# Kernel tuning notes

Hardware: AMD Instinct MI355X
Metric: run time of the kernel (lower is better)

## Reference

```python
import jax, jax.numpy as jnp
import numpy as np

H = 16
D_K = 64
D_V = 64


def setup_inputs() -> dict:
    key = jax.random.key(0)
    k0, k1, k2, k3, k4 = jax.random.split(key, 5)
    n, l, d_model = 4, 2048, 1024
    s = 1.0 / np.sqrt(d_model)
    Z = jax.random.normal(k0, (n, l, d_model), dtype=jnp.float32)
    mask = jnp.ones((n, 1, 1, l), dtype=jnp.int32)
    Wv = jax.random.normal(k1, (d_model, d_model), dtype=jnp.float32) * s
    Wk = jax.random.normal(k2, (d_model, H * D_K), dtype=jnp.float32) * s
    Wq = jax.random.normal(k3, (d_model, H * D_K), dtype=jnp.float32) * s
    Wo = jax.random.normal(k4, (H * D_V, d_model), dtype=jnp.float32) * s
    return {"Z": Z, "mask": mask, "Wv": Wv, "Wk": Wk, "Wq": Wq, "Wo": Wo}


def reference(Z, mask, Wv, Wk, Wq, Wo):
    n, l, d_model = Z.shape
    values = (Z @ Wv).reshape(n, l, H, D_V)
    keys = (Z @ Wk).reshape(n, l, H, D_K)
    queries = (Z @ Wq).reshape(n, l, H, D_K)
    # dense score matrix [n, h, q, k]
    C = jnp.einsum('nqhd,nkhd->nhqk', queries, keys)
    masked_C = jnp.where(mask == 0, -jnp.inf, C)
    idx = jnp.argmax(masked_C, axis=3)          # [n, h, q] hard top-1 index
    # torch einsum 'nhll,nlhd->nlhd' takes the diagonal of the one-hot
    # scattered C_tilde: diag element is C[n,h,l,l] iff argmax at query l is l.
    diag_C = jnp.einsum('nhll->nhl', C)         # [n, h, l]
    w = jnp.where(idx == jnp.arange(l)[None, None, :], diag_C, 0.0)  # [n, h, l]
    y_bar = (w.transpose(0, 2, 1)[..., None] * values).reshape(n, l, H * D_V)
    return y_bar @ Wo
```

## Files before the change

kernel.cpp:

```cpp
#include <hip/hip_runtime.h>
#include <hip/hip_bf16.h>
#include <string.h>

#define NB   4
#define LSEQ 2048
#define DMODEL 1024
#define NHEAD 16
#define DKH  64
#define CAND_CAP 32768

typedef __attribute__((ext_vector_type(8)))  short          short8v;
typedef __attribute__((ext_vector_type(8)))  unsigned short ushort8v;
typedef __attribute__((ext_vector_type(4)))  unsigned int   uint4v;
typedef __attribute__((ext_vector_type(16))) float          f32x16;

__device__ inline unsigned short bf16_rne(float v) {
  unsigned u = __builtin_bit_cast(unsigned, v);
  unsigned r = u + 0x7FFFu + ((u >> 16) & 1u);
  return (unsigned short)(r >> 16);
}
__device__ inline float bf16_to_f32(unsigned short u) {
  return __builtin_bit_cast(float, (unsigned)u << 16);
}
__device__ inline unsigned cvtpk2(float lo, float hi) {
  __hip_bfloat162 t = __float22bfloat162_rn(float2{lo, hi});
  unsigned u;
  memcpy(&u, &t, 4);
  return u;
}

__global__ __launch_bounds__(256) void wconv(
    const float* __restrict__ Wq, const float* __restrict__ Wk,
    unsigned short* __restrict__ WThi) {
  __shared__ float T[64][65];
  const int col0 = blockIdx.x * 64, k0 = blockIdx.y * 64;
  const float* W = (col0 < 1024) ? Wq : Wk;
  const int cl0 = (col0 < 1024) ? col0 : col0 - 1024;
  const int tid = threadIdx.x;
#pragma unroll
  for (int u = 0; u < 16; ++u) {
    int lin = u * 256 + tid;
    int r = lin >> 6, c = lin & 63;
    T[r][c] = W[(size_t)(k0 + r) * 1024 + cl0 + c];
  }
  __syncthreads();
#pragma unroll
  for (int u = 0; u < 16; ++u) {
    int lin = u * 256 + tid;
    int cc = lin >> 6, kk = lin & 63;
    WThi[(size_t)(col0 + cc) * 1024 + k0 + kk] = bf16_rne(T[kk][cc]);
  }
}

__global__ __launch_bounds__(256) void proj_hi(
    const float* __restrict__ Z, const unsigned short* __restrict__ WThi,
    unsigned short* __restrict__ Qhd, unsigned short* __restrict__ Khd) {
  __shared__ unsigned short As[128 * 64];
  __shared__ unsigned short Bs[128 * 64];
  const int tid = threadIdx.x;
  const int lane = tid & 63, w = tid >> 6;
  const int l31 = lane & 31, half = lane >> 5;
  const int wrow = w >> 1, wcol = w & 1;
  const int bid = blockIdx.x;
  const int xcd = bid & 7, t = bid >> 3;
  const int brow = (xcd * 8 + (t & 7)) * 128;
  const int bcol = (t >> 3) * 128;

  int ar[4], as_[4];
#pragma unroll
  for (int u = 0; u < 4; ++u) { int c = u * 256 + tid; ar[u] = c >> 3; as_[u] = c & 7; }

  const float* Zb = Z + (size_t)brow * 1024;
  const unsigned short* Wb = WThi + (size_t)bcol * 1024;

  float4 raf[4][2];
  ushort8v rb[4];
#pragma unroll
  for (int u = 0; u < 4; ++u) {
    const float* p = Zb + (size_t)ar[u] * 1024 + as_[u] * 8;
    raf[u][0] = *(const float4*)p; raf[u][1] = *(const float4*)(p + 4);
    rb[u] = *(const ushort8v*)(Wb + (size_t)ar[u] * 1024 + as_[u] * 8);
  }

  f32x16 acc[2][2];
#pragma unroll
  for (int m = 0; m < 2; ++m)
#pragma unroll
    for (int nf = 0; nf < 2; ++nf)
#pragma unroll
      for (int r = 0; r < 16; ++r) acc[m][nf][r] = 0.f;

  for (int k0 = 0; k0 < 1024; k0 += 64) {
    __syncthreads();
#pragma unroll
    for (int u = 0; u < 4; ++u) {
      uint4v uv;
      uv[0] = cvtpk2(raf[u][0].x, raf[u][0].y);
      uv[1] = cvtpk2(raf[u][0].z, raf[u][0].w);
      uv[2] = cvtpk2(raf[u][1].x, raf[u][1].y);
      uv[3] = cvtpk2(raf[u][1].z, raf[u][1].w);
      ushort8v h8 = __builtin_bit_cast(ushort8v, uv);
      int r = ar[u], s = as_[u];
      *(ushort8v*)((char*)As + r * 128 + ((s ^ (r & 7)) << 4)) = h8;
      *(ushort8v*)((char*)Bs + r * 128 + ((s ^ (r & 7)) << 4)) = rb[u];
    }
    __syncthreads();
    const int kn = k0 + 64;
    if (kn < 1024) {
#pragma unroll
      for (int u = 0; u < 4; ++u) {
        const float* p = Zb + (size_t)ar[u] * 1024 + kn + as_[u] * 8;
        raf[u][0] = *(const float4*)p; raf[u][1] = *(const float4*)(p + 4);
        rb[u] = *(const ushort8v*)(Wb + (size_t)ar[u] * 1024 + kn + as_[u] * 8);
      }
    }
    short8v aH[2][4], bH[2][4];
#pragma unroll
    for (int m = 0; m < 2; ++m) {
      int r = wrow * 64 + m * 32 + l31;
#pragma unroll
      for (int kc = 0; kc < 4; ++kc) {
        int sh = kc * 2 + half;
        aH[m][kc] = *(const short8v*)((char*)As + r * 128 + ((sh ^ (r & 7)) << 4));
      }
    }
#pragma unroll
    for (int nf = 0; nf < 2; ++nf) {
      int r = wcol * 64 + nf * 32 + l31;
#pragma unroll
      for (int kc = 0; kc < 4; ++kc) {
        int sh = kc * 2 + half;
        bH[nf][kc] = *(const short8v*)((char*)Bs + r * 128 + ((sh ^ (r & 7)) << 4));
      }
    }
#pragma unroll
    for (int m = 0; m < 2; ++m)
#pragma unroll
      for (int nf = 0; nf < 2; ++nf)
#pragma unroll
        for (int kc = 0; kc < 4; ++kc)
          acc[m][nf] = __builtin_amdgcn_mfma_f32_32x32x16_bf16(aH[m][kc], bH[nf][kc], acc[m][nf], 0, 0, 0);
  }

  unsigned short* Out;
  int coff;
  if (bcol < 1024) { Out = Qhd; coff = bcol; } else { Out = Khd; coff = bcol - 1024; }
#pragma unroll
  for (int m = 0; m < 2; ++m)
#pragma unroll
    for (int nf = 0; nf < 2; ++nf) {
      int colg = coff + wcol * 64 + nf * 32 + l31;
      int head = colg >> 6, cin = colg & 63;
#pragma unroll
      for (int r = 0; r < 16; ++r) {
        int rowg = brow + wrow * 64 + m * 32 + (r & 3) + 8 * (r >> 2) + 4 * half;
        int n = rowg >> 11, l = rowg & 2047;
        Out[((size_t)(n * 16 + head) * 2048 + l) * 64 + cin] = bf16_rne(acc[m][nf][r]);
      }
    }
}

__global__ __launch_bounds__(256) void score_hi(
    const unsigned short* __restrict__ Qhd, const unsigned short* __restrict__ Khd,
    int* __restrict__ cnt_cand, int* __restrict__ cand) {
  __shared__ unsigned short Ks[2 * 64 * 128];
  const int tid = threadIdx.x;
  const int lane = tid & 63, w = tid >> 6;
  const int l31 = lane & 31, half = lane >> 5;
  const int bid = blockIdx.x;
  const int xcd = bid & 7, j = bid >> 3;
  const int nh = xcd + 8 * (j >> 4);
  const int qi = j & 15;
  const int n = nh >> 4, h = nh & 15;
  const int qw = qi * 128 + w * 32;

  const unsigned short* qrow = Qhd + ((size_t)(nh) * 2048 + qw + l31) * 64;
  short8v aQ[4];
#pragma unroll
  for (int ds = 0; ds < 4; ++ds)
    aQ[ds] = *(const short8v*)(qrow + ds * 16 + 8 * half);

  f32x16 zac;
#pragma unroll
  for (int r = 0; r < 16; ++r) zac[r] = 0.f;

  float maxO[16], diag[16];
#pragma unroll
  for (int r = 0; r < 16; ++r) { maxO[r] = -3.0e38f; diag[r] = -3.0e38f; }

  const unsigned short* kb = Khd + (size_t)nh * 2048 * 64;
  ushort8v rv[4];
#pragma unroll
  for (int u = 0; u < 4; ++u) {
    int c = u * 256 + tid;
    rv[u] = *(const ushort8v*)(kb + (size_t)(c >> 3) * 64 + (c & 7) * 8);
  }

  for (int kt = 0; kt < LSEQ; kt += 128) {
    char* buf = (char*)Ks + ((kt >> 7) & 1) * 16384;
#pragma unroll
    for (int u = 0; u < 4; ++u) {
      int c = u * 256 + tid;
      int pr = c >> 4, sl = c & 15;
      *(ushort8v*)(buf + pr * 256 + ((sl ^ (pr & 15)) << 4)) = rv[u];
    }
    __syncthreads();
    const int ktn = kt + 128;
    if (ktn < LSEQ) {
#pragma unroll
      for (int u = 0; u < 4; ++u) {
        int c = u * 256 + tid;
        rv[u] = *(const ushort8v*)(kb + (size_t)(ktn + (c >> 3)) * 64 + (c & 7) * 8);
      }
    }
    if (kt == qi * 128) {
#pragma unroll
      for (int ct = 0; ct < 4; ++ct) {
        const int rr = ct * 32 + l31;
        const int pr = rr >> 1;
        short8v bh[4];
#pragma unroll
        for (int ds = 0; ds < 4; ++ds) {
          int sl = ((rr & 1) << 3) | (2 * ds + half);
          bh[ds] = *(const short8v*)(buf + pr * 256 + ((sl ^ (pr & 15)) << 4));
        }
        f32x16 acc = __builtin_amdgcn_mfma_f32_32x32x16_bf16(aQ[0], bh[0], zac, 0, 0, 0);
#pragma unroll
        for (int ds = 1; ds < 4; ++ds)
          acc = __builtin_amdgcn_mfma_f32_32x32x16_bf16(aQ[ds], bh[ds], acc, 0, 0, 0);
        if (ct == w) {
#pragma unroll
          for (int r = 0; r < 16; ++r) {
            const int rloc = (r & 3) + 8 * (r >> 2) + 4 * half;
            if (l31 == rloc) diag[r] = acc[r];
            else             maxO[r] = fmaxf(maxO[r], acc[r]);
          }
        } else {
#pragma unroll
          for (int r = 0; r < 16; ++r) maxO[r] = fmaxf(maxO[r], acc[r]);
        }
      }
    } else {
#pragma unroll
      for (int p = 0; p < 2; ++p) {
        const int rrA = (2 * p) * 32 + l31, rrB = (2 * p + 1) * 32 + l31;
        const int prA = rrA >> 1, prB = rrB >> 1;
        short8v bA[4], bB[4];
#pragma unroll
        for (int ds = 0; ds < 4; ++ds) {
          int slA = ((rrA & 1) << 3) | (2 * ds + half);
          int slB = ((rrB & 1) << 3) | (2 * ds + half);
          bA[ds] = *(const short8v*)(buf + prA * 256 + ((slA ^ (prA & 15)) << 4));
          bB[ds] = *(const short8v*)(buf + prB * 256 + ((slB ^ (prB & 15)) << 4));
        }
        f32x16 accA = __builtin_amdgcn_mfma_f32_32x32x16_bf16(aQ[0], bA[0], zac, 0, 0, 0);
        f32x16 accB = __builtin_amdgcn_mfma_f32_32x32x16_bf16(aQ[0], bB[0], zac, 0, 0, 0);
#pragma unroll
        for (int ds = 1; ds < 4; ++ds) {
          accA = __builtin_amdgcn_mfma_f32_32x32x16_bf16(aQ[ds], bA[ds], accA, 0, 0, 0);
          accB = __builtin_amdgcn_mfma_f32_32x32x16_bf16(aQ[ds], bB[ds], accB, 0, 0, 0);
        }
#pragma unroll
        for (int r = 0; r < 16; ++r)
          maxO[r] = fmaxf(fmaxf(accA[r], accB[r]), maxO[r]);
      }
    }
  }

#pragma unroll
  for (int r = 0; r < 16; ++r) {
    float mo = maxO[r], dg = diag[r];
#pragma unroll
    for (int off = 16; off >= 1; off >>= 1) {
      mo = fmaxf(mo, __shfl_xor(mo, off));
      dg = fmaxf(dg, __shfl_xor(dg, off));
    }
    if (l31 == 0) {
      if (dg >= mo - 0.8f) {
        const int q = qw + (r & 3) + 8 * (r >> 2) + 4 * half;
        int slot = atomicAdd(cnt_cand, 1);
        if (slot < CAND_CAP) cand[slot] = (n << 15) | (h << 11) | q;
      }
    }
  }
}

__global__ __launch_bounds__(256) void recheck2(
    const float* __restrict__ Z, const float* __restrict__ Wq,
    const float* __restrict__ Wk, const float* __restrict__ Wv,
    const float* __restrict__ Wo, const unsigned short* __restrict__ Khd,
    const int* __restrict__ cnt_cand, const int* __restrict__ cand,
    float* __restrict__ out) {
  __shared__ float Zs[1024];
  __shared__ float part[4][64];
  __shared__ float Qex[64];
  __shared__ float Kex[64];
  __shared__ float Svals[2048];
  __shared__ float red[4];
  __shared__ int   Elist[64];
  __shared__ int   Ecnt;
  const int tid = threadIdx.x;
  const int lane = tid & 63, w = tid >> 6;
  int nc = *cnt_cand; if (nc > CAND_CAP) nc = CAND_CAP;

  for (int e = blockIdx.x; e < nc; e += gridDim.x) {
    const int pk = cand[e];
    const int n = pk >> 15, h = (pk >> 11) & 15, q = pk & 2047;
    __syncthreads();
#pragma unroll
    for (int u = 0; u < 4; ++u)
      Zs[tid + u * 256] = Z[((size_t)(n * LSEQ + q)) * 1024 + tid + u * 256];
    if (tid == 0) Ecnt = 0;
    __syncthreads();
    {
      int o = tid & 63, seg = tid >> 6;
      float p = 0.f;
      int d0 = seg * 256;
      for (int d = d0; d < d0 + 256; ++d) p += Zs[d] * Wq[(size_t)d * 1024 + h * 64 + o];
      part[seg][o] = p;
    }
    __syncthreads();
    if (tid < 64) Qex[tid] = part[0][tid] + part[1][tid] + part[2][tid] + part[3][tid];
    __syncthreads();
    const unsigned short* kb = Khd + (size_t)(n * 16 + h) * 2048 * 64;
    float mymax = -3.0e38f;
    for (int k = tid; k < LSEQ; k += 256) {
      const unsigned short* kr = kb + (size_t)k * 64;
      float s = 0.f;
#pragma unroll
      for (int jj = 0; jj < 8; ++jj) {
        ushort8v v = *(const ushort8v*)(kr + jj * 8);
#pragma unroll
        for (int ee = 0; ee < 8; ++ee) s += Qex[jj * 8 + ee] * bf16_to_f32(v[ee]);
      }
      Svals[k] = s;
      if (k != q) mymax = fmaxf(mymax, s);
    }
#pragma unroll
    for (int off = 32; off >= 1; off >>= 1) mymax = fmaxf(mymax, __shfl_xor(mymax, off));
    if (lane == 0) red[w] = mymax;
    __syncthreads();
    const float Mt = fmaxf(fmaxf(red[0], red[1]), fmaxf(red[2], red[3]));
    const float Sqt = Svals[q];
    if (Sqt < Mt - 0.4f) continue;
    for (int k = tid; k < LSEQ; k += 256) {
      if (k != q && Svals[k] >= Sqt - 0.4f) {
        int sl = atomicAdd(&Ecnt, 1);
        if (sl < 64) Elist[sl] = k;
      }
    }
    __syncthreads();
    const int nE = (Ecnt < 64) ? Ecnt : 64;
    float Sq_ex = 0.f;
    bool ok = true;
    for (int i = 0; i <= nE; ++i) {
      const int kk = (i == 0) ? q : Elist[i - 1];
      __syncthreads();
#pragma unroll
      for (int u = 0; u < 4; ++u)
        Zs[tid + u * 256] = Z[((size_t)(n * LSEQ + kk)) * 1024 + tid + u * 256];
      __syncthreads();
      {
        int o = tid & 63, seg = tid >> 6;
        float p = 0.f;
        int d0 = seg * 256;
        for (int d = d0; d < d0 + 256; ++d) p += Zs[d] * Wk[(size_t)d * 1024 + h * 64 + o];
        part[seg][o] = p;
      }
      __syncthreads();
      if (tid < 64) Kex[tid] = part[0][tid] + part[1][tid] + part[2][tid] + part[3][tid];
      __syncthreads();
      if (w == 0) {
        float pr = Qex[lane] * Kex[lane];
#pragma unroll
        for (int off = 32; off >= 1; off >>= 1) pr += __shfl_xor(pr, off);
        if (lane == 0) red[0] = pr;
      }
      __syncthreads();
      const float Sk = red[0];
      if (i == 0) Sq_ex = Sk;
      else        ok = ok && (kk < q ? (Sk < Sq_ex) : (Sk <= Sq_ex));
      __syncthreads();
    }
    if (!ok) continue;
    __syncthreads();
#pragma unroll
    for (int u = 0; u < 4; ++u)
      Zs[tid + u * 256] = Z[((size_t)(n * LSEQ + q)) * 1024 + tid + u * 256];
    __syncthreads();
    {
      int o = tid & 63, seg = tid >> 6;
      float p = 0.f;
      int d0 = seg * 256;
      for (int d = d0; d < d0 + 256; ++d) p += Zs[d] * Wv[(size_t)d * 1024 + h * 64 + o];
      part[seg][o] = p;
    }
    __syncthreads();
    if (tid < 64) Kex[tid] = part[0][tid] + part[1][tid] + part[2][tid] + part[3][tid];
    __syncthreads();
    {
      float a4[4] = {0.f, 0.f, 0.f, 0.f};
      const float* wo = Wo + (size_t)h * DKH * DMODEL;
      for (int jj = 0; jj < 64; ++jj) {
        float vj = Kex[jj];
#pragma unroll
        for (int u = 0; u < 4; ++u) a4[u] += vj * wo[(size_t)jj * DMODEL + tid + u * 256];
      }
      float* orow = out + ((size_t)n * LSEQ + q) * DMODEL;
#pragma unroll
      for (int u = 0; u < 4; ++u) atomicAdd(&orow[tid + u * 256], Sq_ex * a4[u]);
    }
  }
}

extern "C" void kernel_launch(void* const* d_in, const int* in_sizes, int n_in,
                              void* d_out, int out_size, void* d_ws, size_t ws_size,
                              hipStream_t stream) {
  const float* Z  = (const float*)d_in[0];
  const float* Wv = (const float*)d_in[2];
  const float* Wk = (const float*)d_in[3];
  const float* Wq = (const float*)d_in[4];
  const float* Wo = (const float*)d_in[5];
  float* out = (float*)d_out;

  int* cnt_cand = (int*)d_ws;
  int* cand = (int*)((char*)d_ws + 64);
  unsigned short* Khd  = (unsigned short*)((char*)d_ws + (size_t)(4 << 20));
  unsigned short* WThi = (unsigned short*)((char*)d_ws + (size_t)(24 << 20));
  unsigned short* Qhd  = (unsigned short*)d_out;

  hipMemsetAsync(d_ws, 0, 64, stream);

  dim3 gw(32, 16);
  wconv<<<gw, 256, 0, stream>>>(Wq, Wk, WThi);

  proj_hi<<<1024, 256, 0, stream>>>(Z, WThi, Qhd, Khd);

  score_hi<<<1024, 256, 0, stream>>>(Qhd, Khd, cnt_cand, cand);

  hipMemsetAsync(d_out, 0, (size_t)out_size * sizeof(float), stream);
  recheck2<<<256, 256, 0, stream>>>(Z, Wq, Wk, Wv, Wo, Khd, cnt_cand, cand, out);
}
```

Before: 179.6 us.

## Pre-convert Z to bf16 and stage GEMM/score tiles via direct global-to-LDS loads

Adds a zconv kernel that converts Z to bf16 once, then rewrites proj_hi to load A/B tiles with global_load_lds (direct global-to-LDS DMA), using a K-step of 32 and a new XOR swizzle. score_hi also drops its register-staged double buffer in favour of direct LDS loads into a single buffer. The goal is to remove the VGPR round trip and in-loop fp32-to-bf16 conversion, and to cut LDS footprint so occupancy can rise. The cost is an extra kernel pass over Z, twice as many sync-bounded iterations in proj_hi, and the loss of load/compute overlap in score_hi.

```diff
diff --git a/kernel.cpp b/kernel.cpp
--- a/kernel.cpp
+++ b/kernel.cpp
@@ -27,6 +27,22 @@
   unsigned u;
   memcpy(&u, &t, 4);
   return u;
+}
+__device__ inline void gload_lds16(const void* g, void* l) {
+  __builtin_amdgcn_global_load_lds((const __attribute__((address_space(1))) void*)g,
+                                   (__attribute__((address_space(3))) void*)l, 16, 0, 0);
+}
+
+__global__ __launch_bounds__(256) void zconv(
+    const float* __restrict__ Z, unsigned short* __restrict__ Zbf) {
+  size_t c = ((size_t)blockIdx.x * 256 + threadIdx.x) * 8;
+  float4 a = *(const float4*)(Z + c), b = *(const float4*)(Z + c + 4);
+  uint4v uv;
+  uv[0] = cvtpk2(a.x, a.y);
+  uv[1] = cvtpk2(a.z, a.w);
+  uv[2] = cvtpk2(b.x, b.y);
+  uv[3] = cvtpk2(b.z, b.w);
+  *(ushort8v*)(Zbf + c) = __builtin_bit_cast(ushort8v, uv);
 }
 
 __global__ __launch_bounds__(256) void wconv(
@@ -53,10 +69,10 @@
 }
 
 __global__ __launch_bounds__(256) void proj_hi(
-    const float* __restrict__ Z, const unsigned short* __restrict__ WThi,
+    const unsigned short* __restrict__ Zbf, const unsigned short* __restrict__ WThi,
     unsigned short* __restrict__ Qhd, unsigned short* __restrict__ Khd) {
-  __shared__ unsigned short As[128 * 64];
-  __shared__ unsigned short Bs[128 * 64];
+  __shared__ unsigned short As[128 * 32];
+  __shared__ unsigned short Bs[128 * 32];
   const int tid = threadIdx.x;
   const int lane = tid & 63, w = tid >> 6;
   const int l31 = lane & 31, half = lane >> 5;
@@ -66,20 +82,14 @@
   const int brow = (xcd * 8 + (t & 7)) * 128;
   const int bcol = (t >> 3) * 128;
 
-  int ar[4], as_[4];
-#pragma unroll
-  for (int u = 0; u < 4; ++u) { int c = u * 256 + tid; ar[u] = c >> 3; as_[u] = c & 7; }
-
-  const float* Zb = Z + (size_t)brow * 1024;
-  const unsigned short* Wb = WThi + (size_t)bcol * 1024;
-
-  float4 raf[4][2];
-  ushort8v rb[4];
-#pragma unroll
-  for (int u = 0; u < 4; ++u) {
-    const float* p = Zb + (size_t)ar[u] * 1024 + as_[u] * 8;
-    raf[u][0] = *(const float4*)p; raf[u][1] = *(const float4*)(p + 4);
-    rb[u] = *(const ushort8v*)(Wb + (size_t)ar[u] * 1024 + as_[u] * 8);
+  int aoff[2], boff[2];
+#pragma unroll
+  for (int u = 0; u < 2; ++u) {
+    int c = u * 256 + w * 64 + lane;
+    int r = c >> 2, sp = c & 3;
+    int s = sp ^ ((r >> 1) & 3);
+    aoff[u] = (brow + r) * 1024 + s * 8;
+    boff[u] = (bcol + r) * 1024 + s * 8;
   }
 
   f32x16 acc[2][2];
@@ -90,47 +100,33 @@
 #pragma unroll
       for (int r = 0; r < 16; ++r) acc[m][nf][r] = 0.f;
 
-  for (int k0 = 0; k0 < 1024; k0 += 64) {
-    __syncthreads();
-#pragma unroll
-    for (int u = 0; u < 4; ++u) {
-      uint4v uv;
-      uv[0] = cvtpk2(raf[u][0].x, raf[u][0].y);
-      uv[1] = cvtpk2(raf[u][0].z, raf[u][0].w);
-      uv[2] = cvtpk2(raf[u][1].x, raf[u][1].y);
-      uv[3] = cvtpk2(raf[u][1].z, raf[u][1].w);
-      ushort8v h8 = __builtin_bit_cast(ushort8v, uv);
-      int r = ar[u], s = as_[u];
-      *(ushort8v*)((char*)As + r * 128 + ((s ^ (r & 7)) << 4)) = h8;
-      *(ushort8v*)((char*)Bs + r * 128 + ((s ^ (r & 7)) << 4)) = rb[u];
-    }
-    __syncthreads();
-    const int kn = k0 + 64;
-    if (kn < 1024) {
-#pragma unroll
-      for (int u = 0; u < 4; ++u) {
-        const float* p = Zb + (size_t)ar[u] * 1024 + kn + as_[u] * 8;
-        raf[u][0] = *(const float4*)p; raf[u][1] = *(const float4*)(p + 4);
-        rb[u] = *(const ushort8v*)(Wb + (size_t)ar[u] * 1024 + kn + as_[u] * 8);
-      }
-    }
-    short8v aH[2][4], bH[2][4];
+  for (int k0 = 0; k0 < 1024; k0 += 32) {
+    __syncthreads();
+#pragma unroll
+    for (int u = 0; u < 2; ++u) {
+      gload_lds16(Zbf  + (size_t)(aoff[u] + k0), (char*)As + u * 4096 + w * 1024);
+      gload_lds16(WThi + (size_t)(boff[u] + k0), (char*)Bs + u * 4096 + w * 1024);
+    }
+    __syncthreads();
+    short8v aH[2][2], bH[2][2];
 #pragma unroll
     for (int m = 0; m < 2; ++m) {
       int r = wrow * 64 + m * 32 + l31;
-#pragma unroll
-      for (int kc = 0; kc < 4; ++kc) {
-        int sh = kc * 2 + half;
-        aH[m][kc] = *(const short8v*)((char*)As + r * 128 + ((sh ^ (r & 7)) << 4));
+      int sw = (r >> 1) & 3;
+#pragma unroll
+      for (int kc = 0; kc < 2; ++kc) {
+        int sl = (kc * 2 + half) ^ sw;
+        aH[m][kc] = *(const short8v*)((const char*)As + r * 64 + sl * 16);
       }
     }
 #pragma unroll
     for (int nf = 0; nf < 2; ++nf) {
       int r = wcol * 64 + nf * 32 + l31;
-#pragma unroll
-      for (int kc = 0; kc < 4; ++kc) {
-        int sh = kc * 2 + half;
-        bH[nf][kc] = *(const short8v*)((char*)Bs + r * 128 + ((sh ^ (r & 7)) << 4));
+      int sw = (r >> 1) & 3;
+#pragma unroll
+      for (int kc = 0; kc < 2; ++kc) {
+        int sl = (kc * 2 + half) ^ sw;
+        bH[nf][kc] = *(const short8v*)((const char*)Bs + r * 64 + sl * 16);
       }
     }
 #pragma unroll
@@ -138,7 +134,7 @@
 #pragma unroll
       for (int nf = 0; nf < 2; ++nf)
 #pragma unroll
-        for (int kc = 0; kc < 4; ++kc)
+        for (int kc = 0; kc < 2; ++kc)
           acc[m][nf] = __builtin_amdgcn_mfma_f32_32x32x16_bf16(aH[m][kc], bH[nf][kc], acc[m][nf], 0, 0, 0);
   }
 
@@ -163,7 +159,7 @@
 __global__ __launch_bounds__(256) void score_hi(
     const unsigned short* __restrict__ Qhd, const unsigned short* __restrict__ Khd,
     int* __restrict__ cnt_cand, int* __restrict__ cand) {
-  __shared__ unsigned short Ks[2 * 64 * 128];
+  __shared__ unsigned short Ks[64 * 128];
   const int tid = threadIdx.x;
   const int lane = tid & 63, w = tid >> 6;
   const int l31 = lane & 31, half = lane >> 5;
@@ -189,30 +185,22 @@
   for (int r = 0; r < 16; ++r) { maxO[r] = -3.0e38f; diag[r] = -3.0e38f; }
 
   const unsigned short* kb = Khd + (size_t)nh * 2048 * 64;
-  ushort8v rv[4];
+  int koff[4];
 #pragma unroll
   for (int u = 0; u < 4; ++u) {
-    int c = u * 256 + tid;
-    rv[u] = *(const ushort8v*)(kb + (size_t)(c >> 3) * 64 + (c & 7) * 8);
+    int c = u * 256 + w * 64 + lane;
+    int pr = c >> 4, sp = c & 15;
+    int ls = sp ^ (pr & 15);
+    koff[u] = (2 * pr + (ls >> 3)) * 64 + (ls & 7) * 8;
   }
 
   for (int kt = 0; kt < LSEQ; kt += 128) {
-    char* buf = (char*)Ks + ((kt >> 7) & 1) * 16384;
-#pragma unroll
-    for (int u = 0; u < 4; ++u) {
-      int c = u * 256 + tid;
-      int pr = c >> 4, sl = c & 15;
-      *(ushort8v*)(buf + pr * 256 + ((sl ^ (pr & 15)) << 4)) = rv[u];
-    }
-    __syncthreads();
-    const int ktn = kt + 128;
-    if (ktn < LSEQ) {
-#pragma unroll
-      for (int u = 0; u < 4; ++u) {
-        int c = u * 256 + tid;
-        rv[u] = *(const ushort8v*)(kb + (size_t)(ktn + (c >> 3)) * 64 + (c & 7) * 8);
-      }
-    }
+    __syncthreads();
+#pragma unroll
+    for (int u = 0; u < 4; ++u)
+      gload_lds16(kb + (size_t)kt * 64 + koff[u], (char*)Ks + u * 4096 + w * 1024);
+    __syncthreads();
+    char* buf = (char*)Ks;
     if (kt == qi * 128) {
 #pragma unroll
       for (int ct = 0; ct < 4; ++ct) {
@@ -427,14 +415,17 @@
   int* cand = (int*)((char*)d_ws + 64);
   unsigned short* Khd  = (unsigned short*)((char*)d_ws + (size_t)(4 << 20));
   unsigned short* WThi = (unsigned short*)((char*)d_ws + (size_t)(24 << 20));
+  unsigned short* Zbf  = (unsigned short*)((char*)d_ws + (size_t)(28 << 20));
   unsigned short* Qhd  = (unsigned short*)d_out;
 
   hipMemsetAsync(d_ws, 0, 64, stream);
+
+  zconv<<<4096, 256, 0, stream>>>(Z, Zbf);
 
   dim3 gw(32, 16);
   wconv<<<gw, 256, 0, stream>>>(Wq, Wk, WThi);
 
-  proj_hi<<<1024, 256, 0, stream>>>(Z, WThi, Qhd, Khd);
+  proj_hi<<<1024, 256, 0, stream>>>(Zbf, WThi, Qhd, Khd);
 
   score_hi<<<1024, 256, 0, stream>>>(Qhd, Khd, cnt_cand, cand);
 
```

After: 186.4 us. +3.7%, slower.
